# Kernel optimization log

Hardware: AMD Instinct MI355X
Metric: run time of the kernel (lower is better)

## Reference

```python
import jax, jax.numpy as jnp
import numpy as np

N, E, F_IN, H, C, G, OUT = 50000, 800000, 128, 4, 64, 64, 16
NEG_SLOPE = 0.2


def _gat_layer(x, src, dst, W, a_src, a_dst, b):
    # x: [N, Fin]; W: [Fin, H*C]; a_src/a_dst: [H, C]; b: [H*C]
    h = (x @ W).reshape(N, H, C)                      # [N,H,C]
    e_src = jnp.einsum('nhc,hc->nh', h, a_src)        # [N,H]
    e_dst = jnp.einsum('nhc,hc->nh', h, a_dst)
    e = jax.nn.leaky_relu(e_src[src] + e_dst[dst], NEG_SLOPE)  # [Etot,H]
    # segment softmax over edges sharing a destination node
    m = jax.ops.segment_max(e, dst, num_segments=N)   # [N,H]
    ex = jnp.exp(e - m[dst])
    s = jax.ops.segment_sum(ex, dst, num_segments=N)  # [N,H]
    alpha = ex / s[dst]                               # [Etot,H]
    msg = h[src] * alpha[:, :, None]                  # [Etot,H,C]
    out = jax.ops.segment_sum(msg, dst, num_segments=N)
    return out.reshape(N, H * C) + b


def setup_inputs() -> dict:
    key = jax.random.key(0)
    ks = jax.random.split(key, 12)
    x = jax.random.normal(ks[0], (N, F_IN), dtype=jnp.float32)
    edge_index = jax.random.randint(ks[1], (2, E), 0, N, dtype=jnp.int64)
    batch = jnp.sort(jax.random.randint(ks[2], (N,), 0, G, dtype=jnp.int64))
    hc = H * C
    W1 = jax.random.normal(ks[3], (F_IN, hc), dtype=jnp.float32) / np.sqrt(F_IN)
    a_src1 = jax.random.normal(ks[4], (H, C), dtype=jnp.float32) / np.sqrt(C)
    a_dst1 = jax.random.normal(ks[5], (H, C), dtype=jnp.float32) / np.sqrt(C)
    b1 = jnp.zeros((hc,), dtype=jnp.float32)
    W2 = jax.random.normal(ks[6], (hc, hc), dtype=jnp.float32) / np.sqrt(hc)
    a_src2 = jax.random.normal(ks[7], (H, C), dtype=jnp.float32) / np.sqrt(C)
    a_dst2 = jax.random.normal(ks[8], (H, C), dtype=jnp.float32) / np.sqrt(C)
    b2 = jnp.zeros((hc,), dtype=jnp.float32)
    Wlin = jax.random.normal(ks[9], (hc, OUT), dtype=jnp.float32) / np.sqrt(hc)
    blin = jnp.zeros((OUT,), dtype=jnp.float32)
    return dict(x=x, edge_index=edge_index, batch=batch,
                W1=W1, a_src1=a_src1, a_dst1=a_dst1, b1=b1,
                W2=W2, a_src2=a_src2, a_dst2=a_dst2, b2=b2,
                Wlin=Wlin, blin=blin)


def reference(x, edge_index, batch, W1, a_src1, a_dst1, b1,
              W2, a_src2, a_dst2, b2, Wlin, blin):
    # add self-loops (PyG GATConv default add_self_loops=True)
    loops = jnp.arange(N, dtype=edge_index.dtype)
    src = jnp.concatenate([edge_index[0], loops])
    dst = jnp.concatenate([edge_index[1], loops])
    h = jax.nn.relu(_gat_layer(x, src, dst, W1, a_src1, a_dst1, b1))
    h = jax.nn.relu(_gat_layer(h, src, dst, W2, a_src2, a_dst2, b2))
    # global mean pool over graphs
    sums = jax.ops.segment_sum(h, batch, num_segments=G)          # [G, H*C]
    cnt = jax.ops.segment_sum(jnp.ones((N,), h.dtype), batch, num_segments=G)
    pooled = sums / jnp.maximum(cnt, 1.0)[:, None]
    return pooled @ Wlin + blin                                    # [G, OUT]
```

## Files before the change

kernel.cpp:

```cpp
#include <hip/hip_runtime.h>
#include <hip/hip_fp16.h>

#define NN   50000
#define EE   800000
#define ETOT 850000
#define FIN  128
#define HC   256
#define NH   4
#define CH   64
#define NG   64
#define NOUT 16
#define NEG_SLOPE 0.2f

#define NBUCK 391
#define BCAP  4096
#define EPB   4096
#define NEB   208

typedef _Float16 f16x8 __attribute__((ext_vector_type(8)));
typedef float    f32x4 __attribute__((ext_vector_type(4)));

__device__ __forceinline__ void sm_combine(float& m, float& s, float om, float os) {
    float M = fmaxf(m, om);
    s = s * __expf(m - M) + os * __expf(om - M);
    m = M;
}

__global__ __launch_bounds__(256) void edge_bucket(const int* __restrict__ ei,
                                                   int* __restrict__ bucket_counts,
                                                   unsigned* __restrict__ buckets) {
    __shared__ int h[NBUCK];
    __shared__ int bb[NBUCK];
    const int tid = threadIdx.x;
    const int e0  = blockIdx.x * EPB;

    for (int t = tid; t < NBUCK; t += 256) h[t] = 0;
    __syncthreads();

    int srcs[16], dsts[16];
#pragma unroll
    for (int k = 0; k < 16; ++k) {
        int i = e0 + k * 256 + tid;
        int s = 0, d = -1;
        if (i < ETOT) {
            s = (i < EE) ? ei[i] : (i - EE);
            d = (i < EE) ? ei[EE + i] : (i - EE);
            atomicAdd(&h[d >> 7], 1);
        }
        srcs[k] = s; dsts[k] = d;
    }
    __syncthreads();

    for (int t = tid; t < NBUCK; t += 256) {
        bb[t] = atomicAdd(&bucket_counts[t], h[t]);
        h[t]  = 0;
    }
    __syncthreads();

#pragma unroll
    for (int k = 0; k < 16; ++k) {
        int d = dsts[k];
        if (d >= 0) {
            int b = d >> 7;
            int r = atomicAdd(&h[b], 1);
            int idx = bb[b] + r;
            if (idx < BCAP)
                buckets[(size_t)b * BCAP + idx] =
                    (unsigned)srcs[k] | ((unsigned)(d & 127) << 16);
        }
    }
}

__global__ __launch_bounds__(512) void bucket_scan(const int* __restrict__ counts,
                                                   int* __restrict__ basep,
                                                   int* __restrict__ rowptr) {
    __shared__ int lds[512];
    const int tid = threadIdx.x;
    int v = (tid < NBUCK) ? counts[tid] : 0;
    lds[tid] = v;
    __syncthreads();
    for (int off = 1; off < 512; off <<= 1) {
        int t = (tid >= off) ? lds[tid - off] : 0;
        __syncthreads();
        lds[tid] += t;
        __syncthreads();
    }
    if (tid < NBUCK) basep[tid] = lds[tid] - v;
    if (tid == 0) rowptr[NN] = ETOT;
}

__global__ __launch_bounds__(256) void bucket_to_csr(const unsigned* __restrict__ buckets,
                                                     const int* __restrict__ bucket_counts,
                                                     const int* __restrict__ bucket_base,
                                                     int* __restrict__ rowptr,
                                                     int* __restrict__ csr) {
    __shared__ int h[128], c[128], sc[128];
    const int b = blockIdx.x, tid = threadIdx.x;
    const int nb   = bucket_counts[b];
    const int base = bucket_base[b];

    if (tid < 128) h[tid] = 0;
    __syncthreads();
    for (int i = tid; i < nb; i += 256) {
        unsigned p = buckets[(size_t)b * BCAP + i];
        atomicAdd(&h[p >> 16], 1);
    }
    __syncthreads();
    if (tid < 128) sc[tid] = h[tid];
    __syncthreads();
    for (int off = 1; off < 128; off <<= 1) {
        int t = (tid < 128 && tid >= off) ? sc[tid - off] : 0;
        __syncthreads();
        if (tid < 128) sc[tid] += t;
        __syncthreads();
    }
    if (tid < 128) {
        int excl = sc[tid] - h[tid];
        c[tid] = excl;
        int node = (b << 7) + tid;
        if (node < NN) rowptr[node] = base + excl;
    }
    __syncthreads();
    for (int i = tid; i < nb; i += 256) {
        unsigned p = buckets[(size_t)b * BCAP + i];
        int pos = atomicAdd(&c[p >> 16], 1);
        csr[base + pos] = (int)(p & 0xFFFFu);
    }
}

__global__ void f32_to_f16_vec(const float* __restrict__ in, __half* __restrict__ out,
                               int n4) {
    int i = blockIdx.x * 256 + threadIdx.x;
    if (i >= n4) return;
    float4 v = *(const float4*)&in[(size_t)i * 4];
    __half h[4] = {__float2half(v.x), __float2half(v.y), __float2half(v.z), __float2half(v.w)};
    *(uint2*)&out[(size_t)i * 4] = *(uint2*)h;
}

__global__ void w_transpose_f16(const float* __restrict__ W, __half* __restrict__ Wt,
                                int K) {
    int idx = blockIdx.x * 256 + threadIdx.x;
    if (idx >= K * HC) return;
    int n = idx / K, k = idx - n * K;
    Wt[idx] = __float2half(W[(size_t)k * HC + n]);
}

__global__ __launch_bounds__(256) void gemm_f16(const __half* __restrict__ A16,
                                                const __half* __restrict__ Bt16,
                                                __half* __restrict__ C16,
                                                const float* __restrict__ a_src,
                                                const float* __restrict__ a_dst,
                                                float* __restrict__ es,
                                                float* __restrict__ ed,
                                                int M, int K) {
    __shared__ char lds[32768];
    const int tid  = threadIdx.x;
    const int m0   = blockIdx.y * 128;
    const int n0   = blockIdx.x * 128;
    const int wid  = tid >> 6, lane = tid & 63;
    const int wr   = wid >> 1, wc = wid & 1;
    const int l15  = lane & 15, l4 = lane >> 4;
    const int trow = tid >> 3;
    const int tcol = (tid & 7) * 8;

    f32x4 acc[4][4] = {};

    for (int k0 = 0; k0 < K; k0 += 64) {
        __syncthreads();
#pragma unroll
        for (int it = 0; it < 4; ++it) {
            int row = trow + it * 32;
            uint4 v = make_uint4(0u, 0u, 0u, 0u);
            int gr = m0 + row;
            if (gr < M) v = *(const uint4*)&A16[(size_t)gr * K + k0 + tcol];
            int off = (row * 128 + tcol * 2) ^ ((row & 7) << 4);
            *(uint4*)(lds + off) = v;
            uint4 w = *(const uint4*)&Bt16[(size_t)(n0 + row) * K + k0 + tcol];
            int offb = 16384 + ((row * 128 + tcol * 2) ^ ((row & 7) << 4));
            *(uint4*)(lds + offb) = w;
        }
        __syncthreads();
#pragma unroll
        for (int ks = 0; ks < 2; ++ks) {
            f16x8 af[4], bf[4];
#pragma unroll
            for (int i = 0; i < 4; ++i) {
                int rowA = wr * 64 + i * 16 + l15;
                int offA = (rowA * 128 + ks * 64 + l4 * 16) ^ ((rowA & 7) << 4);
                af[i] = *(const f16x8*)(lds + offA);
                int rowB = wc * 64 + i * 16 + l15;
                int offB = 16384 + ((rowB * 128 + ks * 64 + l4 * 16) ^ ((rowB & 7) << 4));
                bf[i] = *(const f16x8*)(lds + offB);
            }
#pragma unroll
            for (int i = 0; i < 4; ++i)
#pragma unroll
                for (int j = 0; j < 4; ++j)
                    acc[i][j] = __builtin_amdgcn_mfma_f32_16x16x32_f16(af[i], bf[j], acc[i][j], 0, 0, 0);
        }
    }
#pragma unroll
    for (int i = 0; i < 4; ++i) {
#pragma unroll
        for (int r = 0; r < 4; ++r) {
            int row = m0 + wr * 64 + i * 16 + l4 * 4 + r;
            if (row < M) {
#pragma unroll
                for (int j = 0; j < 4; ++j) {
                    int col = n0 + wc * 64 + j * 16 + l15;
                    C16[(size_t)row * HC + col] = __float2half(acc[i][j][r]);
                }
            }
        }
    }
    const int hd = blockIdx.x * 2 + wc;
    float as_[4], ad_[4];
#pragma unroll
    for (int j = 0; j < 4; ++j) {
        int c = j * 16 + l15;
        as_[j] = a_src[hd * CH + c];
        ad_[j] = a_dst[hd * CH + c];
    }
#pragma unroll
    for (int i = 0; i < 4; ++i) {
#pragma unroll
        for (int r = 0; r < 4; ++r) {
            float ps = 0.f, pd = 0.f;
#pragma unroll
            for (int j = 0; j < 4; ++j) {
                ps = fmaf(acc[i][j][r], as_[j], ps);
                pd = fmaf(acc[i][j][r], ad_[j], pd);
            }
#pragma unroll
            for (int mm = 8; mm; mm >>= 1) {
                ps += __shfl_xor(ps, mm);
                pd += __shfl_xor(pd, mm);
            }
            int row = m0 + wr * 64 + i * 16 + l4 * 4 + r;
            if (l15 == 0 && row < M) {
                es[row * NH + hd] = ps;
                ed[row * NH + hd] = pd;
            }
        }
    }
}

__global__ __launch_bounds__(256) void softmax_alpha(const float* __restrict__ es,
                                                     const float* __restrict__ ed,
                                                     const int* __restrict__ rowptr,
                                                     const int* __restrict__ csr_src,
                                                     __half* __restrict__ alpha16) {
    const int node = blockIdx.x * 4 + (threadIdx.x >> 6);
    const int lane = threadIdx.x & 63;
    if (node >= NN) return;
    const int start = rowptr[node];
    const int deg   = rowptr[node + 1] - start;

    float4 ed4 = *(const float4*)&ed[node * NH];
    float edn[NH] = {ed4.x, ed4.y, ed4.z, ed4.w};

    float m[NH], s[NH];
#pragma unroll
    for (int h = 0; h < NH; ++h) { m[h] = -1e30f; s[h] = 0.f; }

    for (int j = lane; j < deg; j += 64) {
        int src = csr_src[start + j];
        float4 e4 = *(const float4*)&es[src * NH];
        float ev[NH] = {e4.x, e4.y, e4.z, e4.w};
#pragma unroll
        for (int h = 0; h < NH; ++h) {
            float e = ev[h] + edn[h];
            e = (e > 0.f) ? e : NEG_SLOPE * e;
            sm_combine(m[h], s[h], e, 1.0f);
        }
    }
#pragma unroll
    for (int h = 0; h < NH; ++h)
#pragma unroll
        for (int off = 32; off > 0; off >>= 1) {
            float om = __shfl_xor(m[h], off);
            float os = __shfl_xor(s[h], off);
            sm_combine(m[h], s[h], om, os);
        }
    float is[NH];
#pragma unroll
    for (int h = 0; h < NH; ++h) is[h] = 1.0f / s[h];

    for (int j = lane; j < deg; j += 64) {
        int src = csr_src[start + j];
        float4 e4 = *(const float4*)&es[src * NH];
        float ev[NH] = {e4.x, e4.y, e4.z, e4.w};
        __half ah[4];
#pragma unroll
        for (int h = 0; h < NH; ++h) {
            float e = ev[h] + edn[h];
            e = (e > 0.f) ? e : NEG_SLOPE * e;
            ah[h] = __float2half(__expf(e - m[h]) * is[h]);
        }
        *(uint2*)&alpha16[(size_t)(start + j) * NH] = *(uint2*)ah;
    }
}

__global__ __launch_bounds__(256) void gat_gather(const __half* __restrict__ hfeat,
                                                  const __half* __restrict__ alpha16,
                                                  const int* __restrict__ rowptr,
                                                  const int* __restrict__ csr_src,
                                                  const float* __restrict__ bias,
                                                  __half* __restrict__ out16) {
    const int node = blockIdx.x * 4 + (threadIdx.x >> 6);
    const int lane = threadIdx.x & 63;
    if (node >= NN) return;
    const int start = rowptr[node];
    const int deg   = rowptr[node + 1] - start;
    const int hsel  = lane >> 4;

    float4 acc = make_float4(0.f, 0.f, 0.f, 0.f);
    int j = 0;
    for (; j + 7 < deg; j += 8) {
        const int e = start + j;
        int   idx[8];
        float a[8];
        uint2 r[8];
#pragma unroll
        for (int k = 0; k < 8; ++k) idx[k] = csr_src[e + k];
#pragma unroll
        for (int k = 0; k < 8; ++k) a[k] = __half2float(alpha16[(size_t)(e + k) * NH + hsel]);
#pragma unroll
        for (int k = 0; k < 8; ++k) r[k] = *(const uint2*)&hfeat[(size_t)idx[k] * HC + lane * 4];
#pragma unroll
        for (int k = 0; k < 8; ++k) {
            float2 fa = __half22float2(*reinterpret_cast<__half2*>(&r[k].x));
            float2 fb = __half22float2(*reinterpret_cast<__half2*>(&r[k].y));
            acc.x = fmaf(a[k], fa.x, acc.x); acc.y = fmaf(a[k], fa.y, acc.y);
            acc.z = fmaf(a[k], fb.x, acc.z); acc.w = fmaf(a[k], fb.y, acc.w);
        }
    }
    for (; j < deg; ++j) {
        const int e = start + j;
        int s0 = csr_src[e];
        float a0 = __half2float(alpha16[(size_t)e * NH + hsel]);
        uint2 r0 = *(const uint2*)&hfeat[(size_t)s0 * HC + lane * 4];
        float2 f0a = __half22float2(*reinterpret_cast<__half2*>(&r0.x));
        float2 f0b = __half22float2(*reinterpret_cast<__half2*>(&r0.y));
        acc.x = fmaf(a0, f0a.x, acc.x); acc.y = fmaf(a0, f0a.y, acc.y);
        acc.z = fmaf(a0, f0b.x, acc.z); acc.w = fmaf(a0, f0b.y, acc.w);
    }
    float4 b4 = *(const float4*)&bias[lane * 4];
    __half h[4];
    h[0] = __float2half(fmaxf(acc.x + b4.x, 0.f));
    h[1] = __float2half(fmaxf(acc.y + b4.y, 0.f));
    h[2] = __float2half(fmaxf(acc.z + b4.z, 0.f));
    h[3] = __float2half(fmaxf(acc.w + b4.w, 0.f));
    *(uint2*)&out16[(size_t)node * HC + lane * 4] = *(uint2*)h;
}

__global__ __launch_bounds__(256) void pool_sum(const __half* __restrict__ h,
                                                const int* __restrict__ batch,
                                                float* __restrict__ sums) {
    int t  = threadIdx.x;
    int n0 = blockIdx.x * 128;
    if (n0 >= NN) return;
    int cur = batch[n0];
    float acc = 0.f;
    int nend = min(n0 + 128, NN);
    for (int n = n0; n < nend; ++n) {
        int g = batch[n];
        if (g != cur) {
            atomicAdd(&sums[cur * HC + t], acc);
            acc = 0.f; cur = g;
        }
        acc += __half2float(h[(size_t)n * HC + t]);
    }
    atomicAdd(&sums[cur * HC + t], acc);
}

__global__ void batch_bounds(const int* __restrict__ batch,
                             int* __restrict__ beg, int* __restrict__ end) {
    int i = blockIdx.x * 256 + threadIdx.x;
    if (i >= NN) return;
    int g = batch[i];
    if (i == 0      || batch[i - 1] != g) beg[g] = i;
    if (i == NN - 1 || batch[i + 1] != g) end[g] = i + 1;
}

__global__ __launch_bounds__(256) void final_linear(const float* __restrict__ sums,
                                                    const int* __restrict__ beg,
                                                    const int* __restrict__ end,
                                                    const float* __restrict__ Wlin,
                                                    const float* __restrict__ blin,
                                                    float* __restrict__ out) {
    int idx = blockIdx.x * 256 + threadIdx.x;
    if (idx >= NG * NOUT) return;
    int g = idx >> 4, o = idx & 15;
    float cnt = (float)(end[g] - beg[g]);
    float invc = 1.f / fmaxf(cnt, 1.f);
    float acc = 0.f;
    for (int k = 0; k < HC; ++k) acc += sums[g * HC + k] * Wlin[k * NOUT + o];
    out[idx] = acc * invc + blin[o];
}

extern "C" void kernel_launch(void* const* d_in, const int* in_sizes, int n_in,
                              void* d_out, int out_size, void* d_ws, size_t ws_size,
                              hipStream_t stream) {
    const float* x      = (const float*)d_in[0];
    const int*   ei     = (const int*)d_in[1];
    const int*   batch  = (const int*)d_in[2];
    const float* W1     = (const float*)d_in[3];
    const float* a_src1 = (const float*)d_in[4];
    const float* a_dst1 = (const float*)d_in[5];
    const float* b1     = (const float*)d_in[6];
    const float* W2     = (const float*)d_in[7];
    const float* a_src2 = (const float*)d_in[8];
    const float* a_dst2 = (const float*)d_in[9];
    const float* b2     = (const float*)d_in[10];
    const float* Wlin   = (const float*)d_in[11];
    const float* blin   = (const float*)d_in[12];
    float* out = (float*)d_out;

    char* p = (char*)d_ws;
    auto take = [&](size_t bytes) {
        char* r = p;
        p += (bytes + 255) & ~(size_t)255;
        return r;
    };
    __half*   bufT16 = (__half*)take((size_t)NN * HC * 2);
    __half*   bufH16 = (__half*)take((size_t)NN * HC * 2);
    __half*   x16    = (__half*)take((size_t)NN * FIN * 2);
    __half*   w1t    = (__half*)take((size_t)FIN * HC * 2);
    __half*   w2t    = (__half*)take((size_t)HC * HC * 2);
    float*    es     = (float*)take((size_t)NN * NH * 4);
    float*    ed     = (float*)take((size_t)NN * NH * 4);
    int*      rowptr = (int*)take((size_t)(NN + 1) * 4);
    int*      csr    = (int*)take((size_t)ETOT * 4);
    unsigned* buckets= (unsigned*)take((size_t)NBUCK * BCAP * 4);
    int*      bcnt   = (int*)take((size_t)NBUCK * 4);
    int*      bbase  = (int*)take((size_t)NBUCK * 4);
    __half*   albuf16= (__half*)take((size_t)ETOT * NH * 2);
    float*    sums   = (float*)take((size_t)NG * HC * 4);
    int*      gbeg   = (int*)take((size_t)NG * 4);
    int*      gend   = (int*)take((size_t)NG * 4);

    hipMemsetAsync(bcnt, 0, (size_t)NBUCK * 4, stream);
    hipMemsetAsync(sums, 0, (size_t)NG * HC * 4, stream);
    hipMemsetAsync(gbeg, 0, (size_t)NG * 4, stream);
    hipMemsetAsync(gend, 0, (size_t)NG * 4, stream);

    edge_bucket<<<NEB, 256, 0, stream>>>(ei, bcnt, buckets);
    bucket_scan<<<1, 512, 0, stream>>>(bcnt, bbase, rowptr);
    bucket_to_csr<<<NBUCK, 256, 0, stream>>>(buckets, bcnt, bbase, rowptr, csr);
    f32_to_f16_vec<<<(NN * FIN / 4 + 255) / 256, 256, 0, stream>>>(x, x16, NN * FIN / 4);
    w_transpose_f16<<<(FIN * HC + 255) / 256, 256, 0, stream>>>(W1, w1t, FIN);
    w_transpose_f16<<<(HC * HC + 255) / 256, 256, 0, stream>>>(W2, w2t, HC);

    gemm_f16<<<dim3(2, (NN + 127) / 128), 256, 0, stream>>>(x16, w1t, bufT16,
                                                            a_src1, a_dst1, es, ed, NN, FIN);
    softmax_alpha<<<(NN + 3) / 4, 256, 0, stream>>>(es, ed, rowptr, csr, albuf16);
    gat_gather<<<(NN + 3) / 4, 256, 0, stream>>>(bufT16, albuf16, rowptr, csr, b1, bufH16);

    gemm_f16<<<dim3(2, (NN + 127) / 128), 256, 0, stream>>>(bufH16, w2t, bufT16,
                                                            a_src2, a_dst2, es, ed, NN, HC);
    softmax_alpha<<<(NN + 3) / 4, 256, 0, stream>>>(es, ed, rowptr, csr, albuf16);
    gat_gather<<<(NN + 3) / 4, 256, 0, stream>>>(bufT16, albuf16, rowptr, csr, b2, bufH16);

    pool_sum<<<(NN + 127) / 128, 256, 0, stream>>>(bufH16, batch, sums);
    batch_bounds<<<(NN + 255) / 256, 256, 0, stream>>>(batch, gbeg, gend);
    final_linear<<<4, 256, 0, stream>>>(sums, gbeg, gend, Wlin, blin, out);
}
```

Before: 348.1 us.

## Fuse edge softmax into neighbor gather, recompute alpha on the fly

Merges the softmax_alpha and gat_gather kernels into one per-node kernel. The wavefront first computes the per-head max and sum, then recomputes each edge's attention weight while gathering neighbor features, so the fp16 alpha buffer is no longer written and read back and one launch per layer disappears. The gather is also restructured: each half-wavefront handles alternating edges with 16-byte loads and eight channels per lane, and the two halves are combined with a shuffle at the end. In exchange it repeats the es loads and exp computations per edge and leaves half the lanes idle during the epilogue.

After: 291.2 us. -16.4%, faster.

```diff
diff --git a/kernel.cpp b/kernel.cpp
--- a/kernel.cpp
+++ b/kernel.cpp
@@ -245,11 +245,13 @@
     }
 }
 
-__global__ __launch_bounds__(256) void softmax_alpha(const float* __restrict__ es,
-                                                     const float* __restrict__ ed,
-                                                     const int* __restrict__ rowptr,
-                                                     const int* __restrict__ csr_src,
-                                                     __half* __restrict__ alpha16) {
+__global__ __launch_bounds__(256) void gat_fused(const __half* __restrict__ hfeat,
+                                                 const float* __restrict__ es,
+                                                 const float* __restrict__ ed,
+                                                 const int* __restrict__ rowptr,
+                                                 const int* __restrict__ csr_src,
+                                                 const float* __restrict__ bias,
+                                                 __half* __restrict__ out16) {
     const int node = blockIdx.x * 4 + (threadIdx.x >> 6);
     const int lane = threadIdx.x & 63;
     if (node >= NN) return;
@@ -262,7 +264,6 @@
     float m[NH], s[NH];
 #pragma unroll
     for (int h = 0; h < NH; ++h) { m[h] = -1e30f; s[h] = 0.f; }
-
     for (int j = lane; j < deg; j += 64) {
         int src = csr_src[start + j];
         float4 e4 = *(const float4*)&es[src * NH];
@@ -282,76 +283,73 @@
             float os = __shfl_xor(s[h], off);
             sm_combine(m[h], s[h], om, os);
         }
-    float is[NH];
-#pragma unroll
-    for (int h = 0; h < NH; ++h) is[h] = 1.0f / s[h];
-
-    for (int j = lane; j < deg; j += 64) {
-        int src = csr_src[start + j];
-        float4 e4 = *(const float4*)&es[src * NH];
-        float ev[NH] = {e4.x, e4.y, e4.z, e4.w};
-        __half ah[4];
-#pragma unroll
-        for (int h = 0; h < NH; ++h) {
-            float e = ev[h] + edn[h];
-            e = (e > 0.f) ? e : NEG_SLOPE * e;
-            ah[h] = __float2half(__expf(e - m[h]) * is[h]);
-        }
-        *(uint2*)&alpha16[(size_t)(start + j) * NH] = *(uint2*)ah;
-    }
-}
-
-__global__ __launch_bounds__(256) void gat_gather(const __half* __restrict__ hfeat,
-                                                  const __half* __restrict__ alpha16,
-                                                  const int* __restrict__ rowptr,
-                                                  const int* __restrict__ csr_src,
-                                                  const float* __restrict__ bias,
-                                                  __half* __restrict__ out16) {
-    const int node = blockIdx.x * 4 + (threadIdx.x >> 6);
-    const int lane = threadIdx.x & 63;
-    if (node >= NN) return;
-    const int start = rowptr[node];
-    const int deg   = rowptr[node + 1] - start;
-    const int hsel  = lane >> 4;
-
-    float4 acc = make_float4(0.f, 0.f, 0.f, 0.f);
+
+    const int sub = lane >> 5;
+    const int cl  = lane & 31;
+    const int hsel = cl >> 3;
+    const float mh  = m[hsel];
+    const float ish = 1.0f / s[hsel];
+    const float ehn = edn[hsel];
+
+    float acc[8] = {0.f, 0.f, 0.f, 0.f, 0.f, 0.f, 0.f, 0.f};
     int j = 0;
-    for (; j + 7 < deg; j += 8) {
-        const int e = start + j;
-        int   idx[8];
-        float a[8];
-        uint2 r[8];
-#pragma unroll
-        for (int k = 0; k < 8; ++k) idx[k] = csr_src[e + k];
-#pragma unroll
-        for (int k = 0; k < 8; ++k) a[k] = __half2float(alpha16[(size_t)(e + k) * NH + hsel]);
-#pragma unroll
-        for (int k = 0; k < 8; ++k) r[k] = *(const uint2*)&hfeat[(size_t)idx[k] * HC + lane * 4];
-#pragma unroll
-        for (int k = 0; k < 8; ++k) {
-            float2 fa = __half22float2(*reinterpret_cast<__half2*>(&r[k].x));
-            float2 fb = __half22float2(*reinterpret_cast<__half2*>(&r[k].y));
-            acc.x = fmaf(a[k], fa.x, acc.x); acc.y = fmaf(a[k], fa.y, acc.y);
-            acc.z = fmaf(a[k], fb.x, acc.z); acc.w = fmaf(a[k], fb.y, acc.w);
-        }
-    }
-    for (; j < deg; ++j) {
-        const int e = start + j;
-        int s0 = csr_src[e];
-        float a0 = __half2float(alpha16[(size_t)e * NH + hsel]);
-        uint2 r0 = *(const uint2*)&hfeat[(size_t)s0 * HC + lane * 4];
-        float2 f0a = __half22float2(*reinterpret_cast<__half2*>(&r0.x));
-        float2 f0b = __half22float2(*reinterpret_cast<__half2*>(&r0.y));
-        acc.x = fmaf(a0, f0a.x, acc.x); acc.y = fmaf(a0, f0a.y, acc.y);
-        acc.z = fmaf(a0, f0b.x, acc.z); acc.w = fmaf(a0, f0b.y, acc.w);
-    }
-    float4 b4 = *(const float4*)&bias[lane * 4];
-    __half h[4];
-    h[0] = __float2half(fmaxf(acc.x + b4.x, 0.f));
-    h[1] = __float2half(fmaxf(acc.y + b4.y, 0.f));
-    h[2] = __float2half(fmaxf(acc.z + b4.z, 0.f));
-    h[3] = __float2half(fmaxf(acc.w + b4.w, 0.f));
-    *(uint2*)&out16[(size_t)node * HC + lane * 4] = *(uint2*)h;
+    for (; j + 3 < deg; j += 4) {
+        int jj0 = start + j + sub;
+        int jj1 = start + j + 2 + sub;
+        int s0 = csr_src[jj0];
+        int s1 = csr_src[jj1];
+        float e0 = es[s0 * NH + hsel] + ehn;
+        float e1 = es[s1 * NH + hsel] + ehn;
+        e0 = (e0 > 0.f) ? e0 : NEG_SLOPE * e0;
+        e1 = (e1 > 0.f) ? e1 : NEG_SLOPE * e1;
+        float a0 = __expf(e0 - mh) * ish;
+        float a1 = __expf(e1 - mh) * ish;
+        uint4 r0 = *(const uint4*)&hfeat[(size_t)s0 * HC + cl * 8];
+        uint4 r1 = *(const uint4*)&hfeat[(size_t)s1 * HC + cl * 8];
+        const unsigned* w0 = &r0.x;
+        const unsigned* w1 = &r1.x;
+#pragma unroll
+        for (int q = 0; q < 4; ++q) {
+            float2 f0 = __half22float2(*reinterpret_cast<const __half2*>(&w0[q]));
+            float2 f1 = __half22float2(*reinterpret_cast<const __half2*>(&w1[q]));
+            acc[q * 2]     = fmaf(a0, f0.x, acc[q * 2]);
+            acc[q * 2 + 1] = fmaf(a0, f0.y, acc[q * 2 + 1]);
+            acc[q * 2]     = fmaf(a1, f1.x, acc[q * 2]);
+            acc[q * 2 + 1] = fmaf(a1, f1.y, acc[q * 2 + 1]);
+        }
+    }
+    for (; j < deg; j += 2) {
+        int jj = j + sub;
+        if (jj < deg) {
+            int s0 = csr_src[start + jj];
+            float e0 = es[s0 * NH + hsel] + ehn;
+            e0 = (e0 > 0.f) ? e0 : NEG_SLOPE * e0;
+            float a0 = __expf(e0 - mh) * ish;
+            uint4 r0 = *(const uint4*)&hfeat[(size_t)s0 * HC + cl * 8];
+            const unsigned* w0 = &r0.x;
+#pragma unroll
+            for (int q = 0; q < 4; ++q) {
+                float2 f0 = __half22float2(*reinterpret_cast<const __half2*>(&w0[q]));
+                acc[q * 2]     = fmaf(a0, f0.x, acc[q * 2]);
+                acc[q * 2 + 1] = fmaf(a0, f0.y, acc[q * 2 + 1]);
+            }
+        }
+    }
+#pragma unroll
+    for (int q = 0; q < 8; ++q) acc[q] += __shfl_xor(acc[q], 32);
+
+    if (lane < 32) {
+        float4 b0 = *(const float4*)&bias[cl * 8];
+        float4 b1 = *(const float4*)&bias[cl * 8 + 4];
+        const float* bp0 = &b0.x;
+        const float* bp1 = &b1.x;
+        __half h[8];
+#pragma unroll
+        for (int q = 0; q < 4; ++q) h[q]     = __float2half(fmaxf(acc[q]     + bp0[q], 0.f));
+#pragma unroll
+        for (int q = 0; q < 4; ++q) h[4 + q] = __float2half(fmaxf(acc[4 + q] + bp1[q], 0.f));
+        *(uint4*)&out16[(size_t)node * HC + cl * 8] = *(uint4*)h;
+    }
 }
 
 __global__ __launch_bounds__(256) void pool_sum(const __half* __restrict__ h,
@@ -435,7 +433,6 @@
     unsigned* buckets= (unsigned*)take((size_t)NBUCK * BCAP * 4);
     int*      bcnt   = (int*)take((size_t)NBUCK * 4);
     int*      bbase  = (int*)take((size_t)NBUCK * 4);
-    __half*   albuf16= (__half*)take((size_t)ETOT * NH * 2);
     float*    sums   = (float*)take((size_t)NG * HC * 4);
     int*      gbeg   = (int*)take((size_t)NG * 4);
     int*      gend   = (int*)take((size_t)NG * 4);
@@ -454,13 +451,11 @@
 
     gemm_f16<<<dim3(2, (NN + 127) / 128), 256, 0, stream>>>(x16, w1t, bufT16,
                                                             a_src1, a_dst1, es, ed, NN, FIN);
-    softmax_alpha<<<(NN + 3) / 4, 256, 0, stream>>>(es, ed, rowptr, csr, albuf16);
-    gat_gather<<<(NN + 3) / 4, 256, 0, stream>>>(bufT16, albuf16, rowptr, csr, b1, bufH16);
+    gat_fused<<<(NN + 3) / 4, 256, 0, stream>>>(bufT16, es, ed, rowptr, csr, b1, bufH16);
 
     gemm_f16<<<dim3(2, (NN + 127) / 128), 256, 0, stream>>>(bufH16, w2t, bufT16,
                                                             a_src2, a_dst2, es, ed, NN, HC);
-    softmax_alpha<<<(NN + 3) / 4, 256, 0, stream>>>(es, ed, rowptr, csr, albuf16);
-    gat_gather<<<(NN + 3) / 4, 256, 0, stream>>>(bufT16, albuf16, rowptr, csr, b2, bufH16);
+    gat_fused<<<(NN + 3) / 4, 256, 0, stream>>>(bufT16, es, ed, rowptr, csr, b2, bufH16);
 
     pool_sum<<<(NN + 127) / 128, 256, 0, stream>>>(bufH16, batch, sums);
     batch_bounds<<<(NN + 255) / 256, 256, 0, stream>>>(batch, gbeg, gend);
```
